# Performance work log

Hardware: AMD Instinct MI355X
Metric: run time of the kernel (lower is better)

## Reference

```python
import jax, jax.numpy as jnp
import numpy as np

DIM = 512      # model dim
HEADS = 8
DH = DIM // HEADS          # 64, dim_head
M = DIM // 2               # 256, num_landmarks
ITERS = 6                  # pinv_iterations
K = 33                     # residual_conv_kernel (lucidrains default)
B, N = 4, 4096             # N divisible by M -> no padding branch


def setup_inputs() -> dict:
    key = jax.random.key(0)
    ks = jax.random.split(key, 5)
    s = 0.02
    return {
        "x": jax.random.normal(ks[0], (B, N, DIM), jnp.float32),
        "ln_w": jnp.ones((DIM,), jnp.float32),
        "ln_b": jnp.zeros((DIM,), jnp.float32),
        "w_qkv": jax.random.normal(ks[1], (DIM, 3 * HEADS * DH), jnp.float32) * s,
        "w_out": jax.random.normal(ks[2], (HEADS * DH, DIM), jnp.float32) * s,
        "b_out": jnp.zeros((DIM,), jnp.float32),
        "w_conv": jax.random.normal(ks[3], (HEADS, 1, K, 1), jnp.float32) * s,  # depthwise Conv2d (h,1,33,1)
    }


def _moore_penrose_pinv(x, iters=ITERS):
    # Newton-Schulz iterative pseudo-inverse, as in lucidrains nystrom-attention
    abs_x = jnp.abs(x)
    col = abs_x.sum(-1)
    row = abs_x.sum(-2)
    z = jnp.swapaxes(x, -1, -2) / (jnp.max(col) * jnp.max(row))  # global max, matching torch.max
    I = jnp.eye(x.shape[-1], dtype=x.dtype)
    for _ in range(iters):
        xz = x @ z
        z = 0.25 * z @ (13.0 * I - xz @ (15.0 * I - xz @ (7.0 * I - xz)))
    return z


def reference(x, ln_w, ln_b, w_qkv, w_out, b_out, w_conv):
    b, n, d = x.shape
    # LayerNorm (biased variance, eps=1e-5 as torch default)
    mu = jnp.mean(x, -1, keepdims=True)
    var = jnp.mean(jnp.square(x - mu), -1, keepdims=True)
    xn = (x - mu) / jnp.sqrt(var + 1e-5) * ln_w + ln_b

    qkv = xn @ w_qkv                                   # [b,n,3*h*dh]
    q, k, v = jnp.split(qkv, 3, axis=-1)
    split = lambda t: t.reshape(b, n, HEADS, DH).transpose(0, 2, 1, 3)  # [b,h,n,dh]
    q, k, v = split(q), split(k), split(v)
    q = q * (DH ** -0.5)

    l = n // M                                         # tokens per landmark
    q_l = q.reshape(b, HEADS, M, l, DH).mean(axis=3)   # [b,h,m,dh]
    k_l = k.reshape(b, HEADS, M, l, DH).mean(axis=3)

    sim1 = jnp.einsum('bhid,bhjd->bhij', q, k_l)       # [b,h,n,m]
    sim2 = jnp.einsum('bhid,bhjd->bhij', q_l, k_l)     # [b,h,m,m]
    sim3 = jnp.einsum('bhid,bhjd->bhij', q_l, k)       # [b,h,m,n]
    a1 = jax.nn.softmax(sim1, -1)
    a2 = jax.nn.softmax(sim2, -1)
    a3 = jax.nn.softmax(sim3, -1)

    a2_inv = _moore_penrose_pinv(a2)
    out = (a1 @ a2_inv) @ (a3 @ v)                     # [b,h,n,dh]

    # depthwise residual conv over sequence dim (kernel (33,1), groups=heads)
    res = jax.lax.conv_general_dilated(
        v, w_conv, window_strides=(1, 1),
        padding=((K // 2, K // 2), (0, 0)),
        dimension_numbers=('NCHW', 'OIHW', 'NCHW'),
        feature_group_count=HEADS)
    out = out + res

    out = out.transpose(0, 2, 1, 3).reshape(b, n, HEADS * DH)
    out = out @ w_out + b_out
    return x + out
```

## Files before the change

kernel.cpp:

```cpp
#include <hip/hip_runtime.h>
#include <cstdint>

typedef __bf16 bf16;
typedef __bf16 bf16x8 __attribute__((ext_vector_type(8)));
typedef float  f32x4  __attribute__((ext_vector_type(4)));

__device__ __forceinline__ void glds16(const void* g, void* l) {
  __builtin_amdgcn_global_load_lds((const __attribute__((address_space(1))) void*)g,
                                   (__attribute__((address_space(3))) void*)l, 16, 0, 0);
}

__global__ __launch_bounds__(256) void prep_w(const float* __restrict__ wqkv, const float* __restrict__ wout,
                                              bf16* __restrict__ wqkvT, bf16* __restrict__ woutT) {
  int idx = blockIdx.x * 256 + threadIdx.x;
  if (idx < 98304) {
    int r8 = idx & 63, c = idx >> 6;
    bf16 o[8];
#pragma unroll
    for (int e = 0; e < 8; e++) o[e] = (bf16)wqkv[(long)(r8 * 8 + e) * 1536 + c];
    *(uint4*)(wqkvT + (long)c * 512 + r8 * 8) = *(uint4*)o;
  } else {
    int j = idx - 98304;
    int r8 = j & 63, c = j >> 6;
    bf16 o[8];
#pragma unroll
    for (int e = 0; e < 8; e++) o[e] = (bf16)wout[(long)(r8 * 8 + e) * 512 + c];
    *(uint4*)(woutT + (long)c * 512 + r8 * 8) = *(uint4*)o;
  }
}

__global__ __launch_bounds__(64) void ln_kernel(const float* __restrict__ x,
    const float* __restrict__ w, const float* __restrict__ b, bf16* __restrict__ xn) {
  long row = blockIdx.x;
  int t = threadIdx.x;
  const float* rp = x + row * 512 + t * 8;
  float4 p0 = *(const float4*)rp;
  float4 p1 = *(const float4*)(rp + 4);
  float vals[8] = {p0.x, p0.y, p0.z, p0.w, p1.x, p1.y, p1.z, p1.w};
  float s = 0.f, s2 = 0.f;
#pragma unroll
  for (int e = 0; e < 8; e++) { s += vals[e]; s2 += vals[e] * vals[e]; }
#pragma unroll
  for (int o = 32; o > 0; o >>= 1) { s += __shfl_xor(s, o); s2 += __shfl_xor(s2, o); }
  float mu = s * (1.f / 512.f);
  float var = s2 * (1.f / 512.f) - mu * mu;
  float rstd = rsqrtf(var + 1e-5f);
  float4 w0 = *(const float4*)(w + t * 8), w1 = *(const float4*)(w + t * 8 + 4);
  float4 b0 = *(const float4*)(b + t * 8), b1 = *(const float4*)(b + t * 8 + 4);
  float wv[8] = {w0.x, w0.y, w0.z, w0.w, w1.x, w1.y, w1.z, w1.w};
  float bv[8] = {b0.x, b0.y, b0.z, b0.w, b1.x, b1.y, b1.z, b1.w};
  bf16 outv[8];
#pragma unroll
  for (int e = 0; e < 8; e++) outv[e] = (bf16)((vals[e] - mu) * rstd * wv[e] + bv[e]);
  *(uint4*)(xn + row * 512 + t * 8) = *(uint4*)outv;
}

enum { MODE_BF16 = 1, MODE_QKV = 2, MODE_RESID = 3, MODE_XZ = 4, MODE_DIAG = 5, MODE_Y0 = 6, MODE_ZY = 7, MODE_BF16T = 8 };

template <int KDIM, int MODE>
__global__ __launch_bounds__(256) void gemm_ns(
    const bf16* __restrict__ A, const bf16* __restrict__ B, void* __restrict__ C,
    int N, long sA, long sB, long sC, float alpha, float cdiag,
    const float* __restrict__ scal, bf16* __restrict__ aux0, bf16* __restrict__ aux1) {
  constexpr int BM = 64;
  __shared__ __align__(16) bf16 As[BM * KDIM];
  __shared__ __align__(16) bf16 Bs[BM * KDIM];
  const int tid = threadIdx.x, lane = tid & 63, wave = tid >> 6;
  const int quad = lane >> 4, l16 = lane & 15;
  constexpr int LPR = KDIM / 8;
  constexpr int CPW = (BM * KDIM / 512) / 4;
  constexpr int RPC = 64 / LPR;
  const int bm0 = blockIdx.x * BM, bn0 = blockIdx.y * BM;
  const bf16* Ab = A + (long)blockIdx.z * sA;
  const bf16* Bb = B + (long)(MODE == MODE_ZY ? (blockIdx.z & 31) : blockIdx.z) * sB;

  const int rin = lane / LPR, gr = lane % LPR;
#pragma unroll
  for (int t = 0; t < CPW; t++) {
    int seg = wave * CPW + t;
    int row = seg * RPC + rin;
    int scol = 8 * (gr ^ (row & 7));
    glds16(&Ab[(long)(bm0 + row) * KDIM + scol], &As[seg * 512]);
    glds16(&Bb[(long)(bn0 + row) * KDIM + scol], &Bs[seg * 512]);
  }
  __syncthreads();

  f32x4 zero = {0.f, 0.f, 0.f, 0.f};
  f32x4 acc[4];
#pragma unroll
  for (int j = 0; j < 4; j++) acc[j] = zero;
  const int arow = wave * 16 + l16;
  const int aswz = (l16 & 7) * 8;
#pragma unroll
  for (int ki = 0; ki < KDIM / 32; ki++) {
    int cph = (ki * 32 + quad * 8) ^ aswz;
    bf16x8 af = *(const bf16x8*)&As[arow * KDIM + cph];
    bf16x8 bfr[4];
#pragma unroll
    for (int j = 0; j < 4; j++)
      bfr[j] = *(const bf16x8*)&Bs[(j * 16 + l16) * KDIM + cph];
#pragma unroll
    for (int j = 0; j < 4; j++)
      acc[j] = __builtin_amdgcn_mfma_f32_16x16x32_bf16(af, bfr[j], acc[j], 0, 0, 0);
  }

  const long cb = (long)blockIdx.z * sC;
  float rscale = 1.f;
  if (MODE == MODE_Y0) rscale = 1.f / (scal[0] * scal[1]);
#pragma unroll
  for (int j = 0; j < 4; j++)
#pragma unroll
    for (int r = 0; r < 4; r++) {
      int row = bm0 + wave * 16 + quad * 4 + r;
      int col = bn0 + j * 16 + l16;
      float v = acc[j][r] * alpha;
      if (MODE == MODE_BF16) {
        ((bf16*)C)[cb + (long)row * N + col] = (bf16)v;
      } else if (MODE == MODE_Y0) {
        long o = cb + (long)row * N + col;
        float vv = v * rscale;
        aux0[o] = (bf16)vv;
        aux1[o] = (bf16)(((row == col) ? cdiag : 0.f) - vv);
      } else if (MODE == MODE_ZY) {
        long o = cb + (long)row * N + col;
        ((bf16*)C)[o] = (bf16)v;
        if (blockIdx.z >= 32) aux1[o - 2097152] = (bf16)(((row == col) ? cdiag : 0.f) - v);
      } else if (MODE == MODE_DIAG) {
        ((bf16*)C)[cb + (long)row * N + col] = (bf16)(((row == col) ? cdiag : 0.f) - v);
      }
    }
}

template <int BM, int MODE>
__global__ __launch_bounds__(256) void gemm_g(
    const bf16* __restrict__ A, const bf16* __restrict__ B, void* __restrict__ C,
    int N, int K, long sA, long sB, long sC, float alpha, float cdiag,
    const float* __restrict__ resid, const float* __restrict__ bias,
    bf16* __restrict__ aux0, bf16* __restrict__ aux1, bf16* __restrict__ aux2) {
  constexpr int BK = 32, BN = BM;
  __shared__ __align__(16) bf16 As[BM * BK];
  __shared__ __align__(16) bf16 Bs[BN * BK];
  const int tid = threadIdx.x, lane = tid & 63, wave = tid >> 6;
  const int quad = lane >> 4, l16 = lane & 15;
  constexpr int WN = (BN >= 128) ? 2 : 1;
  constexpr int WM = 4 / WN;
  constexpr int TM = BM / (WM * 16), TN = BN / (WN * 16);
  constexpr int ISS = BM / 64;
  const int wm0 = (wave / WN) * (BM / WM);
  const int wn0 = (wave % WN) * (BN / WN);
  const int bm0 = blockIdx.x * BM, bn0 = blockIdx.y * BN;
  const bf16* Ab = A + (long)blockIdx.z * sA;
  const bf16* Bb = B + (long)blockIdx.z * sB;
  const int srow = lane >> 2, scol = (lane & 3) * 8;

  f32x4 zero = {0.f, 0.f, 0.f, 0.f};
  f32x4 acc[TM][TN];
#pragma unroll
  for (int i = 0; i < TM; i++)
#pragma unroll
    for (int j = 0; j < TN; j++) acc[i][j] = zero;

  for (int k0 = 0; k0 < K; k0 += BK) {
#pragma unroll
    for (int t = 0; t < ISS; t++) {
      int seg = wave * ISS + t;
      glds16(&Ab[(long)(bm0 + seg * 16 + srow) * K + k0 + scol], &As[seg * 512]);
      glds16(&Bb[(long)(bn0 + seg * 16 + srow) * K + k0 + scol], &Bs[seg * 512]);
    }
    __syncthreads();
    bf16x8 af[TM], bfr[TN];
#pragma unroll
    for (int i = 0; i < TM; i++)
      af[i] = *(const bf16x8*)&As[(wm0 + i * 16 + l16) * BK + quad * 8];
#pragma unroll
    for (int j = 0; j < TN; j++)
      bfr[j] = *(const bf16x8*)&Bs[(wn0 + j * 16 + l16) * BK + quad * 8];
#pragma unroll
    for (int i = 0; i < TM; i++)
#pragma unroll
      for (int j = 0; j < TN; j++)
        acc[i][j] = __builtin_amdgcn_mfma_f32_16x16x32_bf16(af[i], bfr[j], acc[i][j], 0, 0, 0);
    __syncthreads();
  }

  const long cb = (long)blockIdx.z * sC;
#pragma unroll
  for (int i = 0; i < TM; i++)
#pragma unroll
    for (int j = 0; j < TN; j++)
#pragma unroll
      for (int r = 0; r < 4; r++) {
        int row = bm0 + wm0 + i * 16 + quad * 4 + r;
        int col = bn0 + wn0 + j * 16 + l16;
        float v = acc[i][j][r] * alpha;
        if (MODE == MODE_QKV) {
          int b = row >> 12, n = row & 4095;
          int which = col >> 9, h = (col >> 6) & 7, d = col & 63;
          long o = ((long)(b * 8 + h) * 4096 + n) * 64 + d;
          if (which == 0) aux0[o] = (bf16)(v * 0.125f);
          else if (which == 1) aux1[o] = (bf16)v;
          else aux2[o] = (bf16)v;
        } else {
          long o = (long)row * N + col;
          ((float*)C)[o] = v + bias[col] + resid[o];
        }
      }
}

template <int BM, int BN, bool BT, int MODE>
__global__ __launch_bounds__(256) void gemm_k(
    const bf16* __restrict__ A, const bf16* __restrict__ B, void* __restrict__ C,
    int M, int N, int K, long sA, long sB, long sC, float alpha, float cdiag,
    const float* __restrict__ resid, const float* __restrict__ bias,
    bf16* __restrict__ aux0, bf16* __restrict__ aux1, bf16* __restrict__ aux2) {
  constexpr int BK = 32, LDST = 40;
  __shared__ __align__(16) bf16 As[BM * LDST];
  __shared__ __align__(16) bf16 Bs[BN * LDST];
  const int tid = threadIdx.x, lane = tid & 63, wave = tid >> 6;
  const int quad = lane >> 4, l16 = lane & 15;
  constexpr int WN = (BN >= 128) ? 2 : 1;
  constexpr int WM = 4 / WN;
  constexpr int TM = BM / (WM * 16), TN = BN / (WN * 16);
  const int wm0 = (wave / WN) * (BM / WM);
  const int wn0 = (wave % WN) * (BN / WN);
  const int bm0 = blockIdx.x * BM, bn0 = blockIdx.y * BN;
  const bf16* Ab = A + (long)blockIdx.z * sA;
  const bf16* Bb = B + (long)blockIdx.z * sB;

  f32x4 zero = {0.f, 0.f, 0.f, 0.f};
  f32x4 acc[TM][TN];
#pragma unroll
  for (int i = 0; i < TM; i++)
#pragma unroll
    for (int j = 0; j < TN; j++) acc[i][j] = zero;

  for (int k0 = 0; k0 < K; k0 += BK) {
    for (int c = tid; c < BM * 4; c += 256) {
      int r = c >> 2, cv = (c & 3) * 8;
      *(uint4*)&As[r * LDST + cv] = *(const uint4*)&Ab[(long)(bm0 + r) * K + k0 + cv];
    }
    if (BT) {
      for (int c = tid; c < BN * 4; c += 256) {
        int r = c >> 2, cv = (c & 3) * 8;
        *(uint4*)&Bs[r * LDST + cv] = *(const uint4*)&Bb[(long)(bn0 + r) * K + k0 + cv];
      }
    } else {
      for (int c = tid; c < BN * 4; c += 256) {
        int kk = c / (BN / 8), nv = (c % (BN / 8)) * 8;
        uint4 tmp = *(const uint4*)&Bb[(long)(k0 + kk) * N + bn0 + nv];
        const bf16* tv = (const bf16*)&tmp;
#pragma unroll
        for (int e = 0; e < 8; e++) Bs[(nv + e) * LDST + kk] = tv[e];
      }
    }
    __syncthreads();
    bf16x8 af[TM], bfr[TN];
#pragma unroll
    for (int i = 0; i < TM; i++)
      af[i] = *(const bf16x8*)&As[(wm0 + i * 16 + l16) * LDST + quad * 8];
#pragma unroll
    for (int j = 0; j < TN; j++)
      bfr[j] = *(const bf16x8*)&Bs[(wn0 + j * 16 + l16) * LDST + quad * 8];
#pragma unroll
    for (int i = 0; i < TM; i++)
#pragma unroll
      for (int j = 0; j < TN; j++)
        acc[i][j] = __builtin_amdgcn_mfma_f32_16x16x32_bf16(af[i], bfr[j], acc[i][j], 0, 0, 0);
    __syncthreads();
  }

  const long cb = (long)blockIdx.z * sC;
#pragma unroll
  for (int i = 0; i < TM; i++)
#pragma unroll
    for (int j = 0; j < TN; j++)
#pragma unroll
      for (int r = 0; r < 4; r++) {
        int row = bm0 + wm0 + i * 16 + quad * 4 + r;
        int col = bn0 + wn0 + j * 16 + l16;
        float v = acc[i][j][r] * alpha;
        if (MODE == MODE_BF16) {
          ((bf16*)C)[cb + (long)row * N + col] = (bf16)v;
        } else if (MODE == MODE_BF16T) {
          ((bf16*)C)[cb + (long)col * M + row] = (bf16)v;
        }
      }
}

__global__ __launch_bounds__(256) void lm_kernel(const bf16* __restrict__ q, const bf16* __restrict__ k,
                                                 bf16* __restrict__ ql, bf16* __restrict__ kl) {
  int bh = blockIdx.x, mi = blockIdx.y * 4 + (threadIdx.x >> 6), d = threadIdx.x & 63;
  long base = ((long)bh * 4096 + mi * 16) * 64 + d;
  float sq = 0.f, sk = 0.f;
#pragma unroll
  for (int j = 0; j < 16; j++) { sq += (float)q[base + j * 64]; sk += (float)k[base + j * 64]; }
  long o = ((long)bh * 256 + mi) * 64 + d;
  ql[o] = (bf16)(sq * (1.f / 16.f));
  kl[o] = (bf16)(sk * (1.f / 16.f));
}

__global__ __launch_bounds__(256) void softmax256(bf16* __restrict__ buf) {
  long row = blockIdx.x;
  int t = threadIdx.x, lane = t & 63, wave = t >> 6;
  __shared__ float sm[4];
  float v = (float)buf[row * 256 + t];
  float m = v;
#pragma unroll
  for (int o = 32; o > 0; o >>= 1) m = fmaxf(m, __shfl_xor(m, o));
  if (lane == 0) sm[wave] = m;
  __syncthreads();
  m = fmaxf(fmaxf(sm[0], sm[1]), fmaxf(sm[2], sm[3]));
  float e = __expf(v - m);
  __syncthreads();
  float s = e;
#pragma unroll
  for (int o = 32; o > 0; o >>= 1) s += __shfl_xor(s, o);
  if (lane == 0) sm[wave] = s;
  __syncthreads();
  s = sm[0] + sm[1] + sm[2] + sm[3];
  buf[row * 256 + t] = (bf16)(e / s);
}

__global__ void init_scal(float* scal) { scal[0] = 1.0f; ((int*)scal)[1] = 0; }

__global__ __launch_bounds__(64) void red_col(const bf16* __restrict__ a2h, float* scal) {
  int bh = blockIdx.x;
  int j = blockIdx.y * 64 + threadIdx.x;
  float s = 0.f;
  const bf16* p = a2h + (long)bh * 65536 + j;
  for (int i = 0; i < 256; i++) s += (float)p[i * 256];
  atomicMax((int*)scal + 1, __float_as_int(s));
}

__global__ __launch_bounds__(256) void z0_k(const bf16* __restrict__ a2h,
                                            const float* __restrict__ scal, bf16* __restrict__ z) {
  int bh = blockIdx.x, ti = blockIdx.y;
  int r0 = (ti >> 2) * 64, c0 = (ti & 3) * 64;
  __shared__ __align__(16) bf16 tile[64][72];
  float inv = 1.f / (scal[0] * scal[1]);
  int tid = threadIdx.x;
  const bf16* src = a2h + (long)bh * 65536;
  bf16* dst = z + (long)bh * 65536;
#pragma unroll
  for (int t = 0; t < 2; t++) {
    int i = tid + t * 256;
    int r = i >> 3, c8 = (i & 7) * 8;
    uint4 pk = *(const uint4*)&src[(long)(r0 + r) * 256 + c0 + c8];
    bf16 tmp[8]; *(uint4*)tmp = pk;
    bf16 sc[8];
#pragma unroll
    for (int e = 0; e < 8; e++) sc[e] = (bf16)((float)tmp[e] * inv);
    *(uint4*)&tile[r][c8] = *(uint4*)sc;
  }
  __syncthreads();
#pragma unroll
  for (int t = 0; t < 2; t++) {
    int i = tid + t * 256;
    int jl = i >> 3, c8 = (i & 7) * 8;
    bf16 o[8];
#pragma unroll
    for (int e = 0; e < 8; e++) o[e] = tile[c8 + e][jl];
    *(uint4*)&dst[(long)(c0 + jl) * 256 + r0 + c8] = *(uint4*)o;
  }
}

__global__ __launch_bounds__(256) void f3_partial(const bf16* __restrict__ ql,
    const bf16* __restrict__ k, const bf16* __restrict__ v,
    float* __restrict__ Opart, float* __restrict__ lpart) {
  const int mt = blockIdx.x, ns = blockIdx.y, bh = blockIdx.z;
  const int tid = threadIdx.x, lane = tid & 63, wave = tid >> 6;
  const int quad = lane >> 4, l16 = lane & 15;
  const int wr0 = mt * 128 + wave * 32;
  __shared__ __align__(16) bf16 vT[64][72];
  __shared__ __align__(16) bf16 Pts[4][32][72];

  const bf16* qlb = ql + (long)bh * 16384;
  const bf16* kb  = k + (long)bh * 262144;
  const bf16* vb  = v + (long)bh * 262144;

  bf16x8 aq[2][2];
#pragma unroll
  for (int ti = 0; ti < 2; ti++)
#pragma unroll
    for (int ki = 0; ki < 2; ki++)
      aq[ti][ki] = *(const bf16x8*)&qlb[(wr0 + ti * 16 + l16) * 64 + ki * 32 + quad * 8];

  f32x4 zero = {0.f, 0.f, 0.f, 0.f};
  f32x4 Oacc[2][4];
#pragma unroll
  for (int i = 0; i < 2; i++)
#pragma unroll
    for (int j = 0; j < 4; j++) Oacc[i][j] = zero;
  float lacc[2][4] = {};

  for (int c = 0; c < 8; c++) {
    int n0c = ns * 512 + c * 64;
    __syncthreads();
    for (int i = tid; i < 512; i += 256) {
      int nn = i >> 3, d8 = (i & 7) * 8;
      uint4 pk = *(const uint4*)&vb[(long)(n0c + nn) * 64 + d8];
      const bf16* pv = (const bf16*)&pk;
#pragma unroll
      for (int e = 0; e < 8; e++) vT[d8 + e][nn] = pv[e];
    }
    __syncthreads();

    f32x4 sacc[2][4];
#pragma unroll
    for (int i = 0; i < 2; i++)
#pragma unroll
      for (int j = 0; j < 4; j++) sacc[i][j] = zero;
#pragma unroll
    for (int ki = 0; ki < 2; ki++) {
      bf16x8 bk[4];
#pragma unroll
      for (int tj = 0; tj < 4; tj++)
        bk[tj] = *(const bf16x8*)&kb[(long)(n0c + tj * 16 + l16) * 64 + ki * 32 + quad * 8];
#pragma unroll
      for (int ti = 0; ti < 2; ti++)
#pragma unroll
        for (int tj = 0; tj < 4; tj++)
          sacc[ti][tj] = __builtin_amdgcn_mfma_f32_16x16x32_bf16(aq[ti][ki], bk[tj], sacc[ti][tj], 0, 0, 0);
    }
#pragma unroll
    for (int ti = 0; ti < 2; ti++)
#pragma unroll
      for (int tj = 0; tj < 4; tj++)
#pragma unroll
        for (int r = 0; r < 4; r++) {
          float e = __expf(sacc[ti][tj][r]);
          lacc[ti][r] += e;
          Pts[wave][ti * 16 + quad * 4 + r][tj * 16 + l16] = (bf16)e;
        }
#pragma unroll
    for (int ki = 0; ki < 2; ki++) {
      bf16x8 ap[2], bv[4];
#pragma unroll
      for (int ti = 0; ti < 2; ti++)
        ap[ti] = *(const bf16x8*)&Pts[wave][ti * 16 + l16][ki * 32 + quad * 8];
#pragma unroll
      for (int tj = 0; tj < 4; tj++)
        bv[tj] = *(const bf16x8*)&vT[tj * 16 + l16][ki * 32 + quad * 8];
#pragma unroll
      for (int ti = 0; ti < 2; ti++)
#pragma unroll
        for (int tj = 0; tj < 4; tj++)
          Oacc[ti][tj] = __builtin_amdgcn_mfma_f32_16x16x32_bf16(ap[ti], bv[tj], Oacc[ti][tj], 0, 0, 0);
    }
  }

#pragma unroll
  for (int ti = 0; ti < 2; ti++)
#pragma unroll
    for (int r = 0; r < 4; r++) {
#pragma unroll
      for (int o = 1; o < 16; o <<= 1) lacc[ti][r] += __shfl_xor(lacc[ti][r], o);
    }
  long pb = ((long)bh * 8 + ns) * 256;
#pragma unroll
  for (int ti = 0; ti < 2; ti++)
#pragma unroll
    for (int r = 0; r < 4; r++) {
      int row = wr0 + ti * 16 + quad * 4 + r;
      if (l16 == 0) lpart[pb + row] = lacc[ti][r];
#pragma unroll
      for (int tj = 0; tj < 4; tj++)
        Opart[(pb + row) * 64 + tj * 16 + l16] = Oacc[ti][tj][r];
    }
}

__global__ __launch_bounds__(256) void f3_combine(const float* __restrict__ Opart,
    const float* __restrict__ lpart, bf16* __restrict__ a3v) {
  int row = blockIdx.x * 4 + (threadIdx.x >> 6);
  int d = threadIdx.x & 63;
  int bh = row >> 8, m = row & 255;
  float so = 0.f, sl = 0.f;
#pragma unroll
  for (int s = 0; s < 8; s++) {
    long pb = ((long)bh * 8 + s) * 256 + m;
    so += Opart[pb * 64 + d];
    sl += lpart[pb];
  }
  a3v[(long)row * 64 + d] = (bf16)(so / sl);
}

__global__ __launch_bounds__(256) void f1_attn(const bf16* __restrict__ q,
    const bf16* __restrict__ kl, const bf16* __restrict__ WT, const bf16* __restrict__ v,
    const float* __restrict__ wconv, bf16* __restrict__ xattn) {
  const int nt = blockIdx.x, bh = blockIdx.y;
  const int h = bh & 7, b = bh >> 3, n0 = nt * 64;
  const int tid = threadIdx.x, lane = tid & 63, wave = tid >> 6;
  const int quad = lane >> 4, l16 = lane & 15;
  __shared__ __align__(16) bf16 Pts[64][264];
  __shared__ __align__(16) bf16 vsT[64][104];
  __shared__ float red[4][64];
  __shared__ float linv[64];

  const bf16* qb  = q + (long)bh * 262144;
  const bf16* klb = kl + (long)bh * 16384;
  const bf16* wtb = WT + (long)bh * 16384;
  const bf16* vb  = v + (long)bh * 262144;

  float wreg = (lane < 33) ? wconv[h * 33 + lane] : 0.f;

  for (int i = tid; i < 768; i += 256) {
    int r = i >> 3, d8 = (i & 7) * 8;
    int n = n0 - 16 + r;
    uint4 val = {0u, 0u, 0u, 0u};
    if (n >= 0 && n < 4096) val = *(const uint4*)&vb[(long)n * 64 + d8];
    const bf16* pv = (const bf16*)&val;
#pragma unroll
    for (int e = 0; e < 8; e++) vsT[d8 + e][r] = pv[e];
  }

  f32x4 zero = {0.f, 0.f, 0.f, 0.f};
  f32x4 sacc[4][4];
#pragma unroll
  for (int i = 0; i < 4; i++)
#pragma unroll
    for (int j = 0; j < 4; j++) sacc[i][j] = zero;
#pragma unroll
  for (int ki = 0; ki < 2; ki++) {
    bf16x8 aq[4], bk[4];
#pragma unroll
    for (int ti = 0; ti < 4; ti++)
      aq[ti] = *(const bf16x8*)&qb[(long)(n0 + ti * 16 + l16) * 64 + ki * 32 + quad * 8];
#pragma unroll
    for (int tj = 0; tj < 4; tj++)
      bk[tj] = *(const bf16x8*)&klb[(long)(wave * 64 + tj * 16 + l16) * 64 + ki * 32 + quad * 8];
#pragma unroll
    for (int ti = 0; ti < 4; ti++)
#pragma unroll
      for (int tj = 0; tj < 4; tj++)
        sacc[ti][tj] = __builtin_amdgcn_mfma_f32_16x16x32_bf16(aq[ti], bk[tj], sacc[ti][tj], 0, 0, 0);
  }
  float ps[4][4] = {};
#pragma unroll
  for (int ti = 0; ti < 4; ti++)
#pragma unroll
    for (int tj = 0; tj < 4; tj++)
#pragma unroll
      for (int r = 0; r < 4; r++) {
        float e = __expf(sacc[ti][tj][r]);
        ps[ti][r] += e;
        Pts[ti * 16 + quad * 4 + r][wave * 64 + tj * 16 + l16] = (bf16)e;
      }
#pragma unroll
  for (int ti = 0; ti < 4; ti++)
#pragma unroll
    for (int r = 0; r < 4; r++) {
#pragma unroll
      for (int o = 1; o < 16; o <<= 1) ps[ti][r] += __shfl_xor(ps[ti][r], o);
      if (l16 == 0) red[wave][ti * 16 + quad * 4 + r] = ps[ti][r];
    }
  __syncthreads();
  if (tid < 64) linv[tid] = 1.f / (red[0][tid] + red[1][tid] + red[2][tid] + red[3][tid]);
  __syncthreads();

  const int r0 = wave * 16;
  f32x4 Oacc[4];
#pragma unroll
  for (int j = 0; j < 4; j++) Oacc[j] = zero;
#pragma unroll
  for (int ki = 0; ki < 8; ki++) {
    bf16x8 ap = *(const bf16x8*)&Pts[r0 + l16][ki * 32 + quad * 8];
    bf16x8 bw[4];
#pragma unroll
    for (int tj = 0; tj < 4; tj++)
      bw[tj] = *(const bf16x8*)&wtb[(long)(tj * 16 + l16) * 256 + ki * 32 + quad * 8];
#pragma unroll
    for (int tj = 0; tj < 4; tj++)
      Oacc[tj] = __builtin_amdgcn_mfma_f32_16x16x32_bf16(ap, bw[tj], Oacc[tj], 0, 0, 0);
  }

  f32x4 Cacc[4];
#pragma unroll
  for (int j = 0; j < 4; j++) Cacc[j] = zero;
#pragma unroll
  for (int ki = 0; ki < 3; ki++) {
    if (ki * 32 + 31 < r0 || ki * 32 > r0 + 47) continue;
    bf16x8 av;
#pragma unroll
    for (int j = 0; j < 8; j++) {
      int idx = ki * 32 + quad * 8 + j - r0 - l16;
      float wv = __shfl(wreg, idx & 63);
      av[j] = (idx >= 0 && idx < 33) ? (bf16)wv : (bf16)0.f;
    }
    bf16x8 bv[4];
#pragma unroll
    for (int tj = 0; tj < 4; tj++)
      bv[tj] = *(const bf16x8*)&vsT[tj * 16 + l16][ki * 32 + quad * 8];
#pragma unroll
    for (int tj = 0; tj < 4; tj++)
      Cacc[tj] = __builtin_amdgcn_mfma_f32_16x16x32_bf16(av, bv[tj], Cacc[tj], 0, 0, 0);
  }

#pragma unroll
  for (int rr = 0; rr < 4; rr++) {
    int row = r0 + quad * 4 + rr;
    float inv = linv[row];
    int n = n0 + row;
#pragma unroll
    for (int tj = 0; tj < 4; tj++) {
      int d = tj * 16 + l16;
      xattn[(((long)b * 4096 + n) << 9) + (h << 6) + d] = (bf16)(Oacc[tj][rr] * inv + Cacc[tj][rr]);
    }
  }
}

extern "C" void kernel_launch(void* const* d_in, const int* in_sizes, int n_in,
                              void* d_out, int out_size, void* d_ws, size_t ws_size,
                              hipStream_t stream) {
  (void)in_sizes; (void)n_in; (void)out_size; (void)ws_size;
  const float* x      = (const float*)d_in[0];
  const float* ln_w   = (const float*)d_in[1];
  const float* ln_b   = (const float*)d_in[2];
  const float* w_qkv  = (const float*)d_in[3];
  const float* w_out  = (const float*)d_in[4];
  const float* b_out  = (const float*)d_in[5];
  const float* w_conv = (const float*)d_in[6];
  float* out = (float*)d_out;

  char* ws = (char*)d_ws;
  const size_t MB = 1u << 20;
  bf16* q      = (bf16*)(ws + 0 * MB);
  bf16* k      = (bf16*)(ws + 16 * MB);
  bf16* v      = (bf16*)(ws + 32 * MB);
  bf16* xn     = (bf16*)(ws + 48 * MB);
  bf16* a2_h   = (bf16*)(ws + 48 * MB);
  bf16* pbuf   = (bf16*)(ws + 52 * MB);
  bf16* qbuf   = (bf16*)(ws + 56 * MB);
  bf16* rbuf   = (bf16*)(ws + 60 * MB);
  bf16* bufA   = (bf16*)(ws + 64 * MB);
  bf16* bufB   = (bf16*)(ws + 72 * MB);
  float* Opart = (float*)(ws + 48 * MB);
  float* lpart = (float*)(ws + 72 * MB);
  bf16* xattn  = (bf16*)(ws + 73 * MB);
  bf16* wqkvT  = (bf16*)(ws + 73 * MB);
  bf16* ql     = (bf16*)(ws + 89 * MB);
  bf16* kl     = (bf16*)(ws + 90 * MB);
  bf16* a3v    = (bf16*)(ws + 91 * MB);
  bf16* W      = (bf16*)(ws + 92 * MB);
  bf16* WT     = (bf16*)(ws + 93 * MB);
  bf16* woutT  = (bf16*)(ws + 94 * MB);
  float* scal  = (float*)(ws + 94 * MB + 512 * 1024);
  (void)W;

  prep_w<<<512, 256, 0, stream>>>(w_qkv, w_out, wqkvT, woutT);
  ln_kernel<<<16384, 64, 0, stream>>>(x, ln_w, ln_b, xn);

  gemm_g<128, MODE_QKV><<<dim3(128, 12, 1), 256, 0, stream>>>(
      xn, wqkvT, nullptr, 1536, 512, 0, 0, 0, 1.f, 0.f, nullptr, nullptr, q, k, v);

  lm_kernel<<<dim3(32, 64), 256, 0, stream>>>(q, k, ql, kl);

  gemm_ns<64, MODE_BF16><<<dim3(4, 4, 32), 256, 0, stream>>>(
      ql, kl, a2_h, 256, 16384, 16384, 65536, 1.f, 0.f, nullptr, nullptr, nullptr);
  softmax256<<<8192, 256, 0, stream>>>(a2_h);

  init_scal<<<1, 1, 0, stream>>>(scal);
  red_col<<<dim3(32, 4), 64, 0, stream>>>(a2_h, scal);
  z0_k<<<dim3(32, 16), 256, 0, stream>>>(a2_h, scal, bufA);
  gemm_ns<256, MODE_Y0><<<dim3(4, 4, 32), 256, 0, stream>>>(
      a2_h, a2_h, nullptr, 256, 65536, 65536, 65536, 1.f, 7.f, scal,
      bufA + 2097152, pbuf);

  bf16* cur = bufA;
  bf16* nxt = bufB;
  for (int it = 0; it < 6; it++) {
    gemm_ns<256, MODE_DIAG><<<dim3(4, 4, 32), 256, 0, stream>>>(
        cur + 2097152, pbuf, qbuf, 256, 65536, 65536, 65536, 1.f, 15.f,
        nullptr, nullptr, nullptr);
    gemm_ns<256, MODE_DIAG><<<dim3(4, 4, 32), 256, 0, stream>>>(
        cur + 2097152, qbuf, rbuf, 256, 65536, 65536, 65536, 1.f, 13.f,
        nullptr, nullptr, nullptr);
    if (it < 5) {
      gemm_ns<256, MODE_ZY><<<dim3(4, 4, 64), 256, 0, stream>>>(
          cur, rbuf, nxt, 256, 65536, 65536, 65536, 0.25f, 7.f,
          nullptr, nullptr, pbuf);
    } else {
      gemm_ns<256, MODE_BF16><<<dim3(4, 4, 32), 256, 0, stream>>>(
          cur, rbuf, nxt, 256, 65536, 65536, 65536, 0.25f, 0.f,
          nullptr, nullptr, nullptr);
    }
    bf16* tmp = cur; cur = nxt; nxt = tmp;
  }

  f3_partial<<<dim3(2, 8, 32), 256, 0, stream>>>(ql, k, v, Opart, lpart);
  f3_combine<<<2048, 256, 0, stream>>>(Opart, lpart, a3v);

  gemm_k<64, 64, false, MODE_BF16T><<<dim3(4, 1, 32), 256, 0, stream>>>(
      cur, a3v, WT, 256, 64, 256, 65536, 16384, 16384, 1.f, 0.f, nullptr, nullptr, nullptr, nullptr, nullptr);

  f1_attn<<<dim3(64, 32), 256, 0, stream>>>(q, kl, WT, v, w_conv, xattn);

  gemm_g<128, MODE_RESID><<<dim3(128, 4, 1), 256, 0, stream>>>(
      xattn, woutT, out, 512, 512, 0, 0, 0, 1.f, 0.f, x, b_out, nullptr, nullptr, nullptr);
}
```

Measured before the change: 439.6 us.

## Fuse sim2 GEMM with softmax, swizzle V-transpose LDS, add MFMA priority hints

Replaces the ql·klᵀ GEMM plus a separate softmax pass with one kernel that computes a 64x256 tile per block in registers and applies the row softmax before writing, removing a launch and a round trip of the a2 buffer. The LayerNorm kernel is regrouped to four rows per 256-thread block. The transposed V tiles in LDS get XOR-swizzled column placement to cut bank conflicts. s_setprio is raised around MFMA bursts in the attention kernels. The fused kernel rounds logits to bf16 before softmax, matching the old path, but holds 16 accumulators per thread.

```diff
diff --git a/kernel.cpp b/kernel.cpp
--- a/kernel.cpp
+++ b/kernel.cpp
@@ -29,10 +29,10 @@
   }
 }
 
-__global__ __launch_bounds__(64) void ln_kernel(const float* __restrict__ x,
+__global__ __launch_bounds__(256) void ln_kernel(const float* __restrict__ x,
     const float* __restrict__ w, const float* __restrict__ b, bf16* __restrict__ xn) {
-  long row = blockIdx.x;
-  int t = threadIdx.x;
+  long row = (long)blockIdx.x * 4 + (threadIdx.x >> 6);
+  int t = threadIdx.x & 63;
   const float* rp = x + row * 512 + t * 8;
   float4 p0 = *(const float4*)rp;
   float4 p1 = *(const float4*)(rp + 4);
@@ -129,6 +129,74 @@
         ((bf16*)C)[cb + (long)row * N + col] = (bf16)(((row == col) ? cdiag : 0.f) - v);
       }
     }
+}
+
+__global__ __launch_bounds__(256) void a2_kernel(const bf16* __restrict__ ql,
+    const bf16* __restrict__ kl, bf16* __restrict__ a2h) {
+  __shared__ __align__(16) bf16 As[64 * 64];
+  __shared__ __align__(16) bf16 Bs[256 * 64];
+  const int tid = threadIdx.x, lane = tid & 63, wave = tid >> 6;
+  const int quad = lane >> 4, l16 = lane & 15;
+  const int bm0 = blockIdx.x * 64, bh = blockIdx.y;
+  const bf16* Ab = ql + (long)bh * 16384;
+  const bf16* Bb = kl + (long)bh * 16384;
+
+  const int rin = lane >> 3, gr = lane & 7;
+#pragma unroll
+  for (int t = 0; t < 2; t++) {
+    int seg = wave * 2 + t;
+    int row = seg * 8 + rin;
+    int scol = 8 * (gr ^ (row & 7));
+    glds16(&Ab[(long)(bm0 + row) * 64 + scol], &As[seg * 512]);
+  }
+#pragma unroll
+  for (int t = 0; t < 8; t++) {
+    int seg = wave * 8 + t;
+    int row = seg * 8 + rin;
+    int scol = 8 * (gr ^ (row & 7));
+    glds16(&Bb[(long)row * 64 + scol], &Bs[seg * 512]);
+  }
+  __syncthreads();
+
+  f32x4 zero = {0.f, 0.f, 0.f, 0.f};
+  f32x4 acc[16];
+#pragma unroll
+  for (int j = 0; j < 16; j++) acc[j] = zero;
+  const int arow = wave * 16 + l16;
+  const int aswz = (l16 & 7) * 8;
+#pragma unroll
+  for (int ki = 0; ki < 2; ki++) {
+    int cph = (ki * 32 + quad * 8) ^ aswz;
+    bf16x8 af = *(const bf16x8*)&As[arow * 64 + cph];
+#pragma unroll
+    for (int j = 0; j < 16; j++) {
+      bf16x8 bfr = *(const bf16x8*)&Bs[(j * 16 + l16) * 64 + cph];
+      acc[j] = __builtin_amdgcn_mfma_f32_16x16x32_bf16(af, bfr, acc[j], 0, 0, 0);
+    }
+  }
+
+#pragma unroll
+  for (int r = 0; r < 4; r++) {
+    float vv[16];
+    float m = -3.4e38f;
+#pragma unroll
+    for (int j = 0; j < 16; j++) {
+      vv[j] = (float)(bf16)acc[j][r];
+      m = fmaxf(m, vv[j]);
+    }
+#pragma unroll
+    for (int o = 1; o < 16; o <<= 1) m = fmaxf(m, __shfl_xor(m, o));
+    float s = 0.f;
+#pragma unroll
+    for (int j = 0; j < 16; j++) { vv[j] = __expf(vv[j] - m); s += vv[j]; }
+#pragma unroll
+    for (int o = 1; o < 16; o <<= 1) s += __shfl_xor(s, o);
+    int row = bm0 + wave * 16 + quad * 4 + r;
+    long base = (long)bh * 65536 + (long)row * 256;
+#pragma unroll
+    for (int j = 0; j < 16; j++)
+      a2h[base + j * 16 + l16] = (bf16)(vv[j] / s);
+  }
 }
 
 template <int BM, int MODE>
@@ -299,28 +367,6 @@
   kl[o] = (bf16)(sk * (1.f / 16.f));
 }
 
-__global__ __launch_bounds__(256) void softmax256(bf16* __restrict__ buf) {
-  long row = blockIdx.x;
-  int t = threadIdx.x, lane = t & 63, wave = t >> 6;
-  __shared__ float sm[4];
-  float v = (float)buf[row * 256 + t];
-  float m = v;
-#pragma unroll
-  for (int o = 32; o > 0; o >>= 1) m = fmaxf(m, __shfl_xor(m, o));
-  if (lane == 0) sm[wave] = m;
-  __syncthreads();
-  m = fmaxf(fmaxf(sm[0], sm[1]), fmaxf(sm[2], sm[3]));
-  float e = __expf(v - m);
-  __syncthreads();
-  float s = e;
-#pragma unroll
-  for (int o = 32; o > 0; o >>= 1) s += __shfl_xor(s, o);
-  if (lane == 0) sm[wave] = s;
-  __syncthreads();
-  s = sm[0] + sm[1] + sm[2] + sm[3];
-  buf[row * 256 + t] = (bf16)(e / s);
-}
-
 __global__ void init_scal(float* scal) { scal[0] = 1.0f; ((int*)scal)[1] = 0; }
 
 __global__ __launch_bounds__(64) void red_col(const bf16* __restrict__ a2h, float* scal) {
@@ -400,8 +446,9 @@
       int nn = i >> 3, d8 = (i & 7) * 8;
       uint4 pk = *(const uint4*)&vb[(long)(n0c + nn) * 64 + d8];
       const bf16* pv = (const bf16*)&pk;
-#pragma unroll
-      for (int e = 0; e < 8; e++) vT[d8 + e][nn] = pv[e];
+      int cs = (((nn >> 3) ^ (d8 >> 3)) * 8) + (nn & 7);
+#pragma unroll
+      for (int e = 0; e < 8; e++) vT[d8 + e][cs] = pv[e];
     }
     __syncthreads();
 
@@ -416,11 +463,13 @@
 #pragma unroll
       for (int tj = 0; tj < 4; tj++)
         bk[tj] = *(const bf16x8*)&kb[(long)(n0c + tj * 16 + l16) * 64 + ki * 32 + quad * 8];
+      __builtin_amdgcn_s_setprio(1);
 #pragma unroll
       for (int ti = 0; ti < 2; ti++)
 #pragma unroll
         for (int tj = 0; tj < 4; tj++)
           sacc[ti][tj] = __builtin_amdgcn_mfma_f32_16x16x32_bf16(aq[ti][ki], bk[tj], sacc[ti][tj], 0, 0, 0);
+      __builtin_amdgcn_s_setprio(0);
     }
 #pragma unroll
     for (int ti = 0; ti < 2; ti++)
@@ -439,13 +488,17 @@
       for (int ti = 0; ti < 2; ti++)
         ap[ti] = *(const bf16x8*)&Pts[wave][ti * 16 + l16][ki * 32 + quad * 8];
 #pragma unroll
-      for (int tj = 0; tj < 4; tj++)
-        bv[tj] = *(const bf16x8*)&vT[tj * 16 + l16][ki * 32 + quad * 8];
+      for (int tj = 0; tj < 4; tj++) {
+        int g = (ki * 4 + quad) ^ ((tj * 2 + (l16 >> 3)) & 7);
+        bv[tj] = *(const bf16x8*)&vT[tj * 16 + l16][g * 8];
+      }
+      __builtin_amdgcn_s_setprio(1);
 #pragma unroll
       for (int ti = 0; ti < 2; ti++)
 #pragma unroll
         for (int tj = 0; tj < 4; tj++)
           Oacc[ti][tj] = __builtin_amdgcn_mfma_f32_16x16x32_bf16(ap[ti], bv[tj], Oacc[ti][tj], 0, 0, 0);
+      __builtin_amdgcn_s_setprio(0);
     }
   }
 
@@ -509,8 +562,9 @@
     uint4 val = {0u, 0u, 0u, 0u};
     if (n >= 0 && n < 4096) val = *(const uint4*)&vb[(long)n * 64 + d8];
     const bf16* pv = (const bf16*)&val;
-#pragma unroll
-    for (int e = 0; e < 8; e++) vsT[d8 + e][r] = pv[e];
+    int cs = (((r >> 3) ^ ((d8 >> 3) & 3)) * 8) + (r & 7);
+#pragma unroll
+    for (int e = 0; e < 8; e++) vsT[d8 + e][cs] = pv[e];
   }
 
   f32x4 zero = {0.f, 0.f, 0.f, 0.f};
@@ -528,11 +582,13 @@
 #pragma unroll
     for (int tj = 0; tj < 4; tj++)
       bk[tj] = *(const bf16x8*)&klb[(long)(wave * 64 + tj * 16 + l16) * 64 + ki * 32 + quad * 8];
+    __builtin_amdgcn_s_setprio(1);
 #pragma unroll
     for (int ti = 0; ti < 4; ti++)
 #pragma unroll
       for (int tj = 0; tj < 4; tj++)
         sacc[ti][tj] = __builtin_amdgcn_mfma_f32_16x16x32_bf16(aq[ti], bk[tj], sacc[ti][tj], 0, 0, 0);
+    __builtin_amdgcn_s_setprio(0);
   }
   float ps[4][4] = {};
 #pragma unroll
@@ -568,9 +624,11 @@
 #pragma unroll
     for (int tj = 0; tj < 4; tj++)
       bw[tj] = *(const bf16x8*)&wtb[(long)(tj * 16 + l16) * 256 + ki * 32 + quad * 8];
+    __builtin_amdgcn_s_setprio(1);
 #pragma unroll
     for (int tj = 0; tj < 4; tj++)
       Oacc[tj] = __builtin_amdgcn_mfma_f32_16x16x32_bf16(ap, bw[tj], Oacc[tj], 0, 0, 0);
+    __builtin_amdgcn_s_setprio(0);
   }
 
   f32x4 Cacc[4];
@@ -588,11 +646,15 @@
     }
     bf16x8 bv[4];
 #pragma unroll
-    for (int tj = 0; tj < 4; tj++)
-      bv[tj] = *(const bf16x8*)&vsT[tj * 16 + l16][ki * 32 + quad * 8];
+    for (int tj = 0; tj < 4; tj++) {
+      int g = (ki * 4 + quad) ^ ((tj * 2 + (l16 >> 3)) & 3);
+      bv[tj] = *(const bf16x8*)&vsT[tj * 16 + l16][g * 8];
+    }
+    __builtin_amdgcn_s_setprio(1);
 #pragma unroll
     for (int tj = 0; tj < 4; tj++)
       Cacc[tj] = __builtin_amdgcn_mfma_f32_16x16x32_bf16(av, bv[tj], Cacc[tj], 0, 0, 0);
+    __builtin_amdgcn_s_setprio(0);
   }
 
 #pragma unroll
@@ -647,16 +709,14 @@
   (void)W;
 
   prep_w<<<512, 256, 0, stream>>>(w_qkv, w_out, wqkvT, woutT);
-  ln_kernel<<<16384, 64, 0, stream>>>(x, ln_w, ln_b, xn);
+  ln_kernel<<<4096, 256, 0, stream>>>(x, ln_w, ln_b, xn);
 
   gemm_g<128, MODE_QKV><<<dim3(128, 12, 1), 256, 0, stream>>>(
       xn, wqkvT, nullptr, 1536, 512, 0, 0, 0, 1.f, 0.f, nullptr, nullptr, q, k, v);
 
   lm_kernel<<<dim3(32, 64), 256, 0, stream>>>(q, k, ql, kl);
 
-  gemm_ns<64, MODE_BF16><<<dim3(4, 4, 32), 256, 0, stream>>>(
-      ql, kl, a2_h, 256, 16384, 16384, 65536, 1.f, 0.f, nullptr, nullptr, nullptr);
-  softmax256<<<8192, 256, 0, stream>>>(a2_h);
+  a2_kernel<<<dim3(4, 32), 256, 0, stream>>>(ql, kl, a2_h);
 
   init_scal<<<1, 1, 0, stream>>>(scal);
   red_col<<<dim3(32, 4), 64, 0, stream>>>(a2_h, scal);
```

New measurement: 431.2 us. Within noise of the previous version (-1.9%).
